# Performance work log

Hardware: AMD Instinct MI355X
Metric: run time of the kernel (lower is better)

The kernel has to match this reference:

```python
import jax, jax.numpy as jnp
import numpy as np

BITS = 8
EPS = 1e-5
NUM_HEADS = 16


def quantize_weight(w, eps=EPS):
    # per-tensor abs-mean scale, ternary weights in {-1, 0, 1}
    scale = jnp.maximum(jnp.mean(jnp.abs(w)), eps)
    qw = jnp.clip(jnp.round(w / scale), -1.0, 1.0)
    return qw, scale


def bitlinear158_inference(x, qw, scale, bias=None, bits=BITS, eps=EPS):
    # per-token abs-max activation quantization to [-Q, Q-1]
    q = float(2 ** (bits - 1))
    gamma = jnp.maximum(jnp.max(jnp.abs(x), axis=-1, keepdims=True), eps)
    qx = jnp.clip(jnp.round(x * (q / gamma)), -q, q - 1.0)
    out = jnp.einsum('...i,oi->...o', qx, qw)
    out = out * (scale * gamma / q)
    if bias is not None:
        out = out + bias
    return out


def setup_inputs() -> dict:
    rng = jax.random.key(0)
    ks = jax.random.split(rng, 7)
    B, L, E = 4, 2048, 1024
    return {
        'query': jax.random.normal(ks[0], (B, L, E), jnp.float32),
        'key': jax.random.normal(ks[1], (B, L, E), jnp.float32),
        'value': jax.random.normal(ks[2], (B, L, E), jnp.float32),
        'in_proj_weight': jax.random.normal(ks[3], (3 * E, E), jnp.float32) * 0.02,
        'in_proj_bias': jax.random.normal(ks[4], (3 * E,), jnp.float32) * 0.02,
        'out_proj_weight': jax.random.normal(ks[5], (E, E), jnp.float32) * 0.02,
        'out_proj_bias': jax.random.normal(ks[6], (E,), jnp.float32) * 0.02,
    }


def reference(query, key, value, in_proj_weight, in_proj_bias, out_proj_weight, out_proj_bias):
    B, Lq, E = query.shape
    Lk = key.shape[1]
    H = NUM_HEADS
    D = E // H

    # quantize weights as done at __init__ time
    qw, kw, vw = jnp.split(in_proj_weight, 3, axis=0)  # each [E, E]
    qb, kb, vb = jnp.split(in_proj_bias, 3, axis=0)
    q_qw, q_s = quantize_weight(qw)
    k_qw, k_s = quantize_weight(kw)
    v_qw, v_s = quantize_weight(vw)
    o_qw, o_s = quantize_weight(out_proj_weight)

    # quantized projections [B, L, E]
    q = bitlinear158_inference(query, q_qw, q_s, qb)
    k = bitlinear158_inference(key, k_qw, k_s, kb)
    v = bitlinear158_inference(value, v_qw, v_s, vb)

    # [B, H, L, D]
    q = q.reshape(B, Lq, H, D).transpose(0, 2, 1, 3)
    k = k.reshape(B, Lk, H, D).transpose(0, 2, 1, 3)
    v = v.reshape(B, Lk, H, D).transpose(0, 2, 1, 3)

    scores = jnp.einsum('bhqd,bhkd->bhqk', q, k) / jnp.sqrt(jnp.asarray(D, q.dtype))
    attn = jax.nn.softmax(scores, axis=-1)
    ctx = jnp.einsum('bhqk,bhkd->bhqd', attn, v)  # [B, H, Lq, D]
    ctx = ctx.transpose(0, 2, 1, 3).reshape(B, Lq, E)

    out = bitlinear158_inference(ctx, o_qw, o_s, out_proj_bias)
    return out
```

## Files before the change

### kernel.cpp

```cpp
#include <hip/hip_runtime.h>
#include <cstdint>
#include <cstddef>

#define BB 4
#define LL 2048
#define EE 1024
#define HH 16
#define DD 64
#define TT (BB*LL)
#define EPSF 1e-5f

typedef _Float16 half8 __attribute__((ext_vector_type(8)));
typedef _Float16 half4v __attribute__((ext_vector_type(4)));
typedef float floatx4 __attribute__((ext_vector_type(4)));
typedef float floatx16 __attribute__((ext_vector_type(16)));
typedef int intx4 __attribute__((ext_vector_type(4)));
typedef unsigned int uintx4 __attribute__((ext_vector_type(4)));
typedef unsigned int uint2v __attribute__((ext_vector_type(2)));

__device__ __forceinline__ void gl_lds16(const void* g, void* l) {
    __builtin_amdgcn_global_load_lds(
        (const __attribute__((address_space(1))) void*)g,
        (__attribute__((address_space(3))) void*)l, 16, 0, 0);
}

__device__ __forceinline__ uint32_t pkrtz(float a, float b) {
    return __builtin_bit_cast(uint32_t, __builtin_amdgcn_cvt_pkrtz(a, b));
}

__global__ void k_absum(const float* __restrict__ in_proj,
                        const float* __restrict__ out_proj,
                        double* __restrict__ sums) {
    const int which = blockIdx.y;
    const float4* src = (const float4*)((which < 3) ? (in_proj + (size_t)which * EE * EE)
                                                    : out_proj);
    double loc = 0.0;
    const int n4 = EE * EE / 4;
    for (int i = blockIdx.x * blockDim.x + threadIdx.x; i < n4; i += gridDim.x * blockDim.x) {
        const float4 v = src[i];
        loc += (double)fabsf(v.x); loc += (double)fabsf(v.y);
        loc += (double)fabsf(v.z); loc += (double)fabsf(v.w);
    }
    #pragma unroll
    for (int off = 32; off > 0; off >>= 1) loc += __shfl_down(loc, off, 64);
    __shared__ double red[4];
    const int lane = threadIdx.x & 63, wv = threadIdx.x >> 6;
    if (lane == 0) red[wv] = loc;
    __syncthreads();
    if (threadIdx.x == 0) {
        double tot = red[0] + red[1] + red[2] + red[3];
        atomicAdd(&sums[which], tot);
    }
}

__global__ void k_quantw(const float* __restrict__ in_proj,
                         const float* __restrict__ out_proj,
                         const double* __restrict__ sums,
                         float* __restrict__ scaleF,
                         int8_t* __restrict__ qw) {
    const int idx = blockIdx.x * blockDim.x + threadIdx.x;
    if (idx < 4) scaleF[idx] = fmaxf((float)(sums[idx] * (1.0 / (EE * EE))), EPSF);
    const int which = idx >> 20;
    const float s = fmaxf((float)(sums[which] * (1.0 / (EE * EE))), EPSF);
    const float w = (which < 3) ? in_proj[idx] : out_proj[idx - 3 * EE * EE];
    float q = rintf(w / s);
    q = fminf(fmaxf(q, -1.f), 1.f);
    qw[idx] = (int8_t)q;
}

__device__ __forceinline__ void gammaq_body(const float* __restrict__ x,
                                            float* __restrict__ g,
                                            int8_t* __restrict__ qx) {
    const int wv = threadIdx.x >> 6, lane = threadIdx.x & 63;
    const int tok = blockIdx.x * 4 + wv;
    const float* xp = x + (size_t)tok * EE;
    float4 v[4];
    #pragma unroll
    for (int i = 0; i < 4; i++) v[i] = *(const float4*)(xp + (lane + 64 * i) * 4);
    float m = 0.f;
    #pragma unroll
    for (int i = 0; i < 4; i++)
        m = fmaxf(m, fmaxf(fmaxf(fabsf(v[i].x), fabsf(v[i].y)),
                           fmaxf(fabsf(v[i].z), fabsf(v[i].w))));
    #pragma unroll
    for (int off = 1; off < 64; off <<= 1) m = fmaxf(m, __shfl_xor(m, off, 64));
    const float gg = fmaxf(m, EPSF);
    const float rg = 128.f / gg;
    int8_t* qp = qx + (size_t)tok * EE;
    #pragma unroll
    for (int i = 0; i < 4; i++) {
        char4 c;
        c.x = (int8_t)(int)fminf(fmaxf(rintf(v[i].x * rg), -128.f), 127.f);
        c.y = (int8_t)(int)fminf(fmaxf(rintf(v[i].y * rg), -128.f), 127.f);
        c.z = (int8_t)(int)fminf(fmaxf(rintf(v[i].z * rg), -128.f), 127.f);
        c.w = (int8_t)(int)fminf(fmaxf(rintf(v[i].w * rg), -128.f), 127.f);
        *(char4*)(qp + (lane + 64 * i) * 4) = c;
    }
    if (lane == 0) g[tok] = gg;
}

__global__ __launch_bounds__(256) void k_gammaq3(const float* __restrict__ q,
                                                 const float* __restrict__ k,
                                                 const float* __restrict__ v,
                                                 float* __restrict__ g,
                                                 int8_t* __restrict__ qx) {
    const int y = blockIdx.y;
    const float* src = (y == 0) ? q : (y == 1) ? k : v;
    gammaq_body(src, g + (size_t)y * TT, qx + (size_t)y * TT * EE);
}

__global__ __launch_bounds__(256) void k_gammaq(const float* __restrict__ x,
                                                float* __restrict__ g,
                                                int8_t* __restrict__ qx) {
    gammaq_body(x, g, qx);
}

__global__ __launch_bounds__(256) void k_bitmm(
    const int8_t* __restrict__ qx_all, const float* __restrict__ gam_all,
    const int8_t* __restrict__ qw_all, const float* __restrict__ scaleF,
    const float* __restrict__ in_proj_b, const float* __restrict__ out_proj_b,
    float* __restrict__ outF, _Float16* __restrict__ outH_all,
    int wbase, float qpre) {
    __shared__ __align__(16) int8_t smem[65536];
    _Float16 (*Vt)[136] = (_Float16(*)[136])smem;

    const int nz = (wbase == 0) ? 3 : 1;
    const int bid = blockIdx.x;
    const int xcd = bid & 7;
    const int idx = bid >> 3;
    const int per = 8 * nz;
    const int xl = idx / per;
    const int rem = idx - xl * per;
    const int y = rem & 7;
    const int z = rem >> 3;
    const int t0 = (xcd * 8 + xl) * 128;
    const int o0 = y * 128;
    const int widx = wbase + z;

    const int8_t* qx = qx_all + (size_t)widx * TT * EE;
    const int8_t* qw = qw_all + (size_t)widx * EE * EE;
    const float* gam = gam_all + (size_t)widx * TT;
    const float* bias = (widx < 3) ? (in_proj_b + widx * EE) : out_proj_b;
    _Float16* outH = outH_all + (size_t)widx * TT * EE;
    const float pre = (widx == 0) ? qpre : 1.0f;
    const int tid = threadIdx.x;
    const int wv = tid >> 6, lane = tid & 63;
    const int quad = lane >> 4, l16 = lane & 15;
    const int wm = wv & 1, wn = wv >> 1;
    const int srow = lane >> 3, schunk = lane & 7;

    intx4 acc[4][4];
    #pragma unroll
    for (int i = 0; i < 4; i++)
        #pragma unroll
        for (int j = 0; j < 4; j++) acc[i][j] = (intx4){0, 0, 0, 0};

    #pragma unroll
    for (int p = 0; p < 4; p++) {
        const int g = wv * 4 + p;
        const int c = schunk ^ srow ^ (g & 7);
        const int row = g * 8 + srow;
        gl_lds16(qx + (size_t)(t0 + row) * EE + c * 16, smem + (size_t)(g * 8) * 128);
        gl_lds16(qw + (size_t)(o0 + row) * EE + c * 16, smem + 32768 + (size_t)(g * 8) * 128);
    }
    __syncthreads();

    for (int k0 = 0; k0 < EE; k0 += 128) {
        const int cur = (k0 >> 7) & 1;
        int8_t (*As)[128] = (int8_t(*)[128])(smem + cur * 16384);
        int8_t (*Bs)[128] = (int8_t(*)[128])(smem + 32768 + cur * 16384);

        if (k0 + 128 < EE) {
            int8_t* Asn = smem + (cur ^ 1) * 16384;
            int8_t* Bsn = smem + 32768 + (cur ^ 1) * 16384;
            const int kn = k0 + 128;
            #pragma unroll
            for (int p = 0; p < 4; p++) {
                const int g = wv * 4 + p;
                const int c = schunk ^ srow ^ (g & 7);
                const int row = g * 8 + srow;
                gl_lds16(qx + (size_t)(t0 + row) * EE + kn + c * 16, Asn + (size_t)(g * 8) * 128);
                gl_lds16(qw + (size_t)(o0 + row) * EE + kn + c * 16, Bsn + (size_t)(g * 8) * 128);
            }
        }

        #pragma unroll
        for (int kk = 0; kk < 2; kk++) {
            intx4 af[4], bf[4];
            #pragma unroll
            for (int s4 = 0; s4 < 4; s4++) {
                const int mR = (l16 & 7) ^ ((s4 * 2 + (l16 >> 3)) & 7);
                const int ph = ((kk * 4 + quad) ^ mR) * 16;
                af[s4] = *(const intx4*)&As[wm * 64 + s4 * 16 + l16][ph];
                bf[s4] = *(const intx4*)&Bs[wn * 64 + s4 * 16 + l16][ph];
            }
            __builtin_amdgcn_s_setprio(1);
            #pragma unroll
            for (int sm = 0; sm < 4; sm++)
                #pragma unroll
                for (int sn = 0; sn < 4; sn++)
                    acc[sm][sn] = __builtin_amdgcn_mfma_i32_16x16x64_i8(
                        af[sm], bf[sn], acc[sm][sn], 0, 0, 0);
            __builtin_amdgcn_s_setprio(0);
        }
        __syncthreads();
    }

    const float s = scaleF[widx];
    if (widx == 2) {
        #pragma unroll
        for (int sm = 0; sm < 4; sm++) {
            const int tl = wm * 64 + sm * 16 + quad * 4;
            float mr[4];
            #pragma unroll
            for (int r = 0; r < 4; r++) mr[r] = s * gam[t0 + tl + r] * 0.0078125f;
            #pragma unroll
            for (int sn = 0; sn < 4; sn++) {
                const int ol = wn * 64 + sn * 16 + l16;
                const float b = bias[o0 + ol];
                half4v hv;
                #pragma unroll
                for (int r = 0; r < 4; r++)
                    hv[r] = (_Float16)((float)acc[sm][sn][r] * mr[r] + b);
                *(half4v*)&Vt[ol][tl] = hv;
            }
        }
        __syncthreads();
        const int ol2 = tid >> 1, tc0 = (tid & 1) * 64;
        const int og = o0 + ol2, hh = og >> 6, dd = og & 63;
        const int bb = t0 >> 11, l0 = t0 & (LL - 1);
        _Float16* dst = outH + ((size_t)(bb * HH + hh) * DD + dd) * LL + l0 + tc0;
        #pragma unroll
        for (int i = 0; i < 8; i++)
            *(half8*)(dst + i * 8) = *(const half8*)&Vt[ol2][tc0 + i * 8];
        return;
    }
    #pragma unroll
    for (int sm = 0; sm < 4; sm++) {
        #pragma unroll
        for (int r = 0; r < 4; r++) {
            const int t = t0 + wm * 64 + sm * 16 + quad * 4 + r;
            const float mr = s * gam[t] * 0.0078125f;
            const int b_ = t >> 11, l_ = t & (LL - 1);
            #pragma unroll
            for (int sn = 0; sn < 4; sn++) {
                const int o = o0 + wn * 64 + sn * 16 + l16;
                const float val = (float)acc[sm][sn][r] * mr + bias[o];
                if (widx == 3) {
                    outF[(size_t)t * EE + o] = val;
                } else {
                    const int h_ = o >> 6, d_ = o & 63;
                    outH[((size_t)(b_ * HH + h_) * LL + l_) * DD + d_] = (_Float16)(val * pre);
                }
            }
        }
    }
}

__global__ __launch_bounds__(256, 4) void k_attn5(const _Float16* __restrict__ Q,
                                                  const _Float16* __restrict__ K,
                                                  const _Float16* __restrict__ Vt,
                                                  float* __restrict__ ctx) {
    __shared__ __align__(16) _Float16 Ksh[2][64][64];
    __shared__ __align__(16) _Float16 Vtsh[2][64][64];
    const int tid = threadIdx.x;
    const int wv = tid >> 6, lane = tid & 63;
    const int l32 = lane & 31, h2 = lane >> 5;
    const int bid = blockIdx.x;
    const int xcd = bid & 7, j = bid >> 3;
    const int bh = (xcd << 3) | (j >> 4);
    const int qblk = j & 15;
    const int b_ = bh >> 4, h_ = bh & 15;
    const int q0 = qblk * 128 + wv * 32;
    const int srow = lane >> 3, schunk = lane & 7;

    const _Float16* Qb = Q + (size_t)bh * LL * DD;
    const _Float16* Kb = K + (size_t)bh * LL * DD;
    const _Float16* Vtb = Vt + (size_t)bh * DD * LL;

    half8 qf[4];
    #pragma unroll
    for (int ds = 0; ds < 4; ds++)
        qf[ds] = *(const half8*)(Qb + (size_t)(q0 + l32) * DD + ds * 16 + h2 * 8);

    floatx16 acc[2], accl, zv;
    #pragma unroll
    for (int r = 0; r < 16; r++) { acc[0][r] = 0.f; acc[1][r] = 0.f; accl[r] = 0.f; zv[r] = 0.f; }
    half8 ones;
    #pragma unroll
    for (int r = 0; r < 8; r++) ones[r] = (_Float16)1.0f;

    {
        #pragma unroll
        for (int u = 0; u < 2; u++) {
            const int g = wv * 2 + u;
            const int c = schunk ^ srow ^ (g & 7);
            const int row = g * 8 + srow;
            gl_lds16(Kb + (size_t)row * DD + c * 8, &Ksh[0][g * 8][0]);
            gl_lds16(Vtb + (size_t)row * LL + c * 8, &Vtsh[0][g * 8][0]);
        }
    }
    __syncthreads();

    for (int kt = 0; kt < LL; kt += 64) {
        const int cur = (kt >> 6) & 1;

        if (kt + 64 < LL) {
            const int nkt = kt + 64;
            #pragma unroll
            for (int u = 0; u < 2; u++) {
                const int g = wv * 2 + u;
                const int c = schunk ^ srow ^ (g & 7);
                const int row = g * 8 + srow;
                gl_lds16(Kb + (size_t)(nkt + row) * DD + c * 8, &Ksh[cur ^ 1][g * 8][0]);
                gl_lds16(Vtb + (size_t)row * LL + nkt + c * 8, &Vtsh[cur ^ 1][g * 8][0]);
            }
        }

        half8 pa[4];
        #pragma unroll
        for (int ks = 0; ks < 2; ks++) {
            const int rowK = ks * 32 + l32;
            const int mK = (l32 & 7) ^ ((ks * 4 + (l32 >> 3)) & 7);
            __builtin_amdgcn_s_setprio(1);
            floatx16 sc;
            {
                const half8 kf = *(const half8*)&Ksh[cur][rowK][((2 * 0 + h2) ^ mK) * 8];
                sc = __builtin_amdgcn_mfma_f32_32x32x16_f16(kf, qf[0], zv, 0, 0, 0);
            }
            #pragma unroll
            for (int ds = 1; ds < 4; ds++) {
                const half8 kf = *(const half8*)&Ksh[cur][rowK][((2 * ds + h2) ^ mK) * 8];
                sc = __builtin_amdgcn_mfma_f32_32x32x16_f16(kf, qf[ds], sc, 0, 0, 0);
            }
            __builtin_amdgcn_s_setprio(0);
            float p[16];
            #pragma unroll
            for (int r = 0; r < 16; r++) p[r] = __builtin_amdgcn_exp2f(sc[r]);
            uint32_t u_[4][2];
            #pragma unroll
            for (int c4 = 0; c4 < 4; c4++) {
                u_[c4][0] = pkrtz(p[4 * c4 + 0], p[4 * c4 + 1]);
                u_[c4][1] = pkrtz(p[4 * c4 + 2], p[4 * c4 + 3]);
            }
            #pragma unroll
            for (int mm = 0; mm < 2; mm++) {
                uint2v s0 = __builtin_amdgcn_permlane32_swap(
                    u_[2 * mm][0], u_[2 * mm + 1][0], false, false);
                uint2v s1 = __builtin_amdgcn_permlane32_swap(
                    u_[2 * mm][1], u_[2 * mm + 1][1], false, false);
                uintx4 w;
                w[0] = s0[0]; w[1] = s1[0]; w[2] = s0[1]; w[3] = s1[1];
                union { uintx4 u; half8 h; } cv; cv.u = w;
                pa[ks * 2 + mm] = cv.h;
            }
        }

        __builtin_amdgcn_s_setprio(1);
        #pragma unroll
        for (int kb = 0; kb < 4; kb++) {
            #pragma unroll
            for (int sd = 0; sd < 2; sd++) {
                const int rowV = sd * 32 + l32;
                const int mV = (l32 & 7) ^ ((sd * 4 + (l32 >> 3)) & 7);
                const half8 vf = *(const half8*)&Vtsh[cur][rowV][((2 * kb + h2) ^ mV) * 8];
                acc[sd] = __builtin_amdgcn_mfma_f32_32x32x16_f16(pa[kb], vf, acc[sd], 0, 0, 0);
            }
            accl = __builtin_amdgcn_mfma_f32_32x32x16_f16(pa[kb], ones, accl, 0, 0, 0);
        }
        __builtin_amdgcn_s_setprio(0);

        __syncthreads();
    }

    #pragma unroll
    for (int r = 0; r < 16; r++) {
        const int qrow = (r & 3) + 8 * (r >> 2) + 4 * h2;
        const float iv = 1.f / accl[r];
        float* cp = ctx + ((size_t)b_ * LL + q0 + qrow) * EE + h_ * DD + l32;
        cp[0]  = acc[0][r] * iv;
        cp[32] = acc[1][r] * iv;
    }
}

extern "C" void kernel_launch(void* const* d_in, const int* in_sizes, int n_in,
                              void* d_out, int out_size, void* d_ws, size_t ws_size,
                              hipStream_t stream) {
    const float* query      = (const float*)d_in[0];
    const float* key        = (const float*)d_in[1];
    const float* value      = (const float*)d_in[2];
    const float* in_proj_w  = (const float*)d_in[3];
    const float* in_proj_b  = (const float*)d_in[4];
    const float* out_proj_w = (const float*)d_in[5];
    const float* out_proj_b = (const float*)d_in[6];
    float* out = (float*)d_out;

    char* ws = (char*)d_ws;
    double*   sums   = (double*)ws;
    float*    scaleF = (float*)(ws + 32);
    float*    gbuf   = (float*)(ws + 256);
    int8_t*   qw8    = (int8_t*)(ws + (size_t)1  * 1024 * 1024);
    int8_t*   qx8    = (int8_t*)(ws + (size_t)8  * 1024 * 1024);
    _Float16* Qh     = (_Float16*)(ws + (size_t)40 * 1024 * 1024);
    _Float16* Kh     = Qh + (size_t)TT * EE;
    _Float16* Vth    = Kh + (size_t)TT * EE;
    float*    ctx    = out;

    const float QPRE = 0.18033688011112042f;

    hipMemsetAsync(sums, 0, 32, stream);
    k_absum<<<dim3(256, 4), 256, 0, stream>>>(in_proj_w, out_proj_w, sums);
    k_quantw<<<(4 * EE * EE) / 256, 256, 0, stream>>>(in_proj_w, out_proj_w, sums, scaleF, qw8);
    k_gammaq3<<<dim3(TT / 4, 3), 256, 0, stream>>>(query, key, value, gbuf, qx8);

    k_bitmm<<<dim3(64 * 8 * 3), 256, 0, stream>>>(
        qx8, gbuf, qw8, scaleF, in_proj_b, out_proj_b, nullptr, Qh, 0, QPRE);

    k_attn5<<<dim3((LL / 128) * BB * HH), 256, 0, stream>>>(Qh, Kh, Vth, ctx);

    k_gammaq<<<TT / 4, 256, 0, stream>>>(ctx, gbuf + 3 * TT, qx8 + 3 * (size_t)TT * EE);
    k_bitmm<<<dim3(64 * 8), 256, 0, stream>>>(
        qx8, gbuf, qw8, scaleF, in_proj_b, out_proj_b, out, Qh, 3, QPRE);
}
```

Baseline: 333.9 us.

## Software-pipeline attention loop: overlap next QK and softmax with previous PV

Restructures the attention inner loop so that the QK^T MFMAs for tile k are issued together with the PV MFMAs for tile k-1, with exp/pack softmax done afterwards. A triple-buffered V tile in a unified LDS array replaces the double-buffered K/V arrays, and the swizzled LDS offsets are precomputed once per thread. The aim is to hide the exp/permlane latency behind matrix work and interleave the two independent MFMA chains. The cost is more LDS (five 64x64 tiles), which lowers the occupancy target from 4 to 3 blocks per CU, and higher register pressure from keeping the previous P fragments live.

```diff
diff --git a/kernel.cpp b/kernel.cpp
--- a/kernel.cpp
+++ b/kernel.cpp
@@ -257,12 +257,11 @@
     }
 }
 
-__global__ __launch_bounds__(256, 4) void k_attn5(const _Float16* __restrict__ Q,
+__global__ __launch_bounds__(256, 3) void k_attn5(const _Float16* __restrict__ Q,
                                                   const _Float16* __restrict__ K,
                                                   const _Float16* __restrict__ Vt,
                                                   float* __restrict__ ctx) {
-    __shared__ __align__(16) _Float16 Ksh[2][64][64];
-    __shared__ __align__(16) _Float16 Vtsh[2][64][64];
+    __shared__ __align__(16) _Float16 sm[5 * 64 * 64];
     const int tid = threadIdx.x;
     const int wv = tid >> 6, lane = tid & 63;
     const int l32 = lane & 31, h2 = lane >> 5;
@@ -283,95 +282,128 @@
     for (int ds = 0; ds < 4; ds++)
         qf[ds] = *(const half8*)(Qb + (size_t)(q0 + l32) * DD + ds * 16 + h2 * 8);
 
+    int offX[2][4];
+    #pragma unroll
+    for (int h = 0; h < 2; h++) {
+        const int mx = (l32 & 7) ^ ((h * 4 + (l32 >> 3)) & 7);
+        #pragma unroll
+        for (int jj = 0; jj < 4; jj++)
+            offX[h][jj] = (h * 32 + l32) * 64 + (((2 * jj + h2) ^ mx) * 8);
+    }
+
     floatx16 acc[2], accl, zv;
     #pragma unroll
     for (int r = 0; r < 16; r++) { acc[0][r] = 0.f; acc[1][r] = 0.f; accl[r] = 0.f; zv[r] = 0.f; }
     half8 ones;
     #pragma unroll
     for (int r = 0; r < 8; r++) ones[r] = (_Float16)1.0f;
-
+    half8 paP[4];
+
+#define STAGE_T(kt_, koff_, voff_)                                                   \
+    {                                                                                \
+        _Pragma("unroll")                                                            \
+        for (int u = 0; u < 2; u++) {                                                \
+            const int g = wv * 2 + u;                                                \
+            const int c = schunk ^ srow ^ (g & 7);                                   \
+            const int row = g * 8 + srow;                                            \
+            gl_lds16(Kb + (size_t)((kt_) + row) * DD + c * 8, sm + (koff_) + g * 8 * 64); \
+            gl_lds16(Vtb + (size_t)row * LL + (kt_) + c * 8, sm + (voff_) + g * 8 * 64);  \
+        }                                                                            \
+    }
+
+#define QK_T(koff_)                                                                  \
+    {                                                                                \
+        const _Float16* kb_ = sm + (koff_);                                          \
+        sc0 = __builtin_amdgcn_mfma_f32_32x32x16_f16(                                \
+            *(const half8*)(kb_ + offX[0][0]), qf[0], zv, 0, 0, 0);                  \
+        sc1 = __builtin_amdgcn_mfma_f32_32x32x16_f16(                                \
+            *(const half8*)(kb_ + offX[1][0]), qf[0], zv, 0, 0, 0);                  \
+        _Pragma("unroll")                                                            \
+        for (int ds = 1; ds < 4; ds++) {                                             \
+            sc0 = __builtin_amdgcn_mfma_f32_32x32x16_f16(                            \
+                *(const half8*)(kb_ + offX[0][ds]), qf[ds], sc0, 0, 0, 0);           \
+            sc1 = __builtin_amdgcn_mfma_f32_32x32x16_f16(                            \
+                *(const half8*)(kb_ + offX[1][ds]), qf[ds], sc1, 0, 0, 0);           \
+        }                                                                            \
+    }
+
+#define PV_T(voff_)                                                                  \
+    {                                                                                \
+        const _Float16* vb_ = sm + (voff_);                                          \
+        _Pragma("unroll")                                                            \
+        for (int kb = 0; kb < 4; kb++) {                                             \
+            acc[0] = __builtin_amdgcn_mfma_f32_32x32x16_f16(                         \
+                paP[kb], *(const half8*)(vb_ + offX[0][kb]), acc[0], 0, 0, 0);       \
+            acc[1] = __builtin_amdgcn_mfma_f32_32x32x16_f16(                         \
+                paP[kb], *(const half8*)(vb_ + offX[1][kb]), acc[1], 0, 0, 0);       \
+            accl = __builtin_amdgcn_mfma_f32_32x32x16_f16(paP[kb], ones, accl, 0, 0, 0); \
+        }                                                                            \
+    }
+
+#define SMAX_HALF(sc_, ks_)                                                          \
+    {                                                                                \
+        float p[16];                                                                 \
+        _Pragma("unroll")                                                            \
+        for (int r = 0; r < 16; r++) p[r] = __builtin_amdgcn_exp2f(sc_[r]);          \
+        uint32_t u_[4][2];                                                           \
+        _Pragma("unroll")                                                            \
+        for (int c4 = 0; c4 < 4; c4++) {                                             \
+            u_[c4][0] = pkrtz(p[4 * c4 + 0], p[4 * c4 + 1]);                         \
+            u_[c4][1] = pkrtz(p[4 * c4 + 2], p[4 * c4 + 3]);                         \
+        }                                                                            \
+        _Pragma("unroll")                                                            \
+        for (int mm = 0; mm < 2; mm++) {                                             \
+            uint2v s0 = __builtin_amdgcn_permlane32_swap(                            \
+                u_[2 * mm][0], u_[2 * mm + 1][0], false, false);                     \
+            uint2v s1 = __builtin_amdgcn_permlane32_swap(                            \
+                u_[2 * mm][1], u_[2 * mm + 1][1], false, false);                     \
+            uintx4 w;                                                                \
+            w[0] = s0[0]; w[1] = s1[0]; w[2] = s0[1]; w[3] = s1[1];                  \
+            union { uintx4 u; half8 h; } cv; cv.u = w;                               \
+            paP[(ks_) * 2 + mm] = cv.h;                                              \
+        }                                                                            \
+    }
+
+    STAGE_T(0, 0, 8192);
+    __syncthreads();
+
+    int vprev = 8192, vcurr = 8192 + 4096, vnext = 8192 + 8192;
+
+    STAGE_T(64, 4096, vcurr);
     {
-        #pragma unroll
-        for (int u = 0; u < 2; u++) {
-            const int g = wv * 2 + u;
-            const int c = schunk ^ srow ^ (g & 7);
-            const int row = g * 8 + srow;
-            gl_lds16(Kb + (size_t)row * DD + c * 8, &Ksh[0][g * 8][0]);
-            gl_lds16(Vtb + (size_t)row * LL + c * 8, &Vtsh[0][g * 8][0]);
-        }
+        floatx16 sc0, sc1;
+        __builtin_amdgcn_s_setprio(1);
+        QK_T(0);
+        __builtin_amdgcn_s_setprio(0);
+        SMAX_HALF(sc0, 0);
+        SMAX_HALF(sc1, 1);
     }
     __syncthreads();
 
-    for (int kt = 0; kt < LL; kt += 64) {
+    for (int kt = 64; kt < LL; kt += 64) {
         const int cur = (kt >> 6) & 1;
-
-        if (kt + 64 < LL) {
-            const int nkt = kt + 64;
-            #pragma unroll
-            for (int u = 0; u < 2; u++) {
-                const int g = wv * 2 + u;
-                const int c = schunk ^ srow ^ (g & 7);
-                const int row = g * 8 + srow;
-                gl_lds16(Kb + (size_t)(nkt + row) * DD + c * 8, &Ksh[cur ^ 1][g * 8][0]);
-                gl_lds16(Vtb + (size_t)row * LL + nkt + c * 8, &Vtsh[cur ^ 1][g * 8][0]);
-            }
-        }
-
-        half8 pa[4];
-        #pragma unroll
-        for (int ks = 0; ks < 2; ks++) {
-            const int rowK = ks * 32 + l32;
-            const int mK = (l32 & 7) ^ ((ks * 4 + (l32 >> 3)) & 7);
-            __builtin_amdgcn_s_setprio(1);
-            floatx16 sc;
-            {
-                const half8 kf = *(const half8*)&Ksh[cur][rowK][((2 * 0 + h2) ^ mK) * 8];
-                sc = __builtin_amdgcn_mfma_f32_32x32x16_f16(kf, qf[0], zv, 0, 0, 0);
-            }
-            #pragma unroll
-            for (int ds = 1; ds < 4; ds++) {
-                const half8 kf = *(const half8*)&Ksh[cur][rowK][((2 * ds + h2) ^ mK) * 8];
-                sc = __builtin_amdgcn_mfma_f32_32x32x16_f16(kf, qf[ds], sc, 0, 0, 0);
-            }
-            __builtin_amdgcn_s_setprio(0);
-            float p[16];
-            #pragma unroll
-            for (int r = 0; r < 16; r++) p[r] = __builtin_amdgcn_exp2f(sc[r]);
-            uint32_t u_[4][2];
-            #pragma unroll
-            for (int c4 = 0; c4 < 4; c4++) {
-                u_[c4][0] = pkrtz(p[4 * c4 + 0], p[4 * c4 + 1]);
-                u_[c4][1] = pkrtz(p[4 * c4 + 2], p[4 * c4 + 3]);
-            }
-            #pragma unroll
-            for (int mm = 0; mm < 2; mm++) {
-                uint2v s0 = __builtin_amdgcn_permlane32_swap(
-                    u_[2 * mm][0], u_[2 * mm + 1][0], false, false);
-                uint2v s1 = __builtin_amdgcn_permlane32_swap(
-                    u_[2 * mm][1], u_[2 * mm + 1][1], false, false);
-                uintx4 w;
-                w[0] = s0[0]; w[1] = s1[0]; w[2] = s0[1]; w[3] = s1[1];
-                union { uintx4 u; half8 h; } cv; cv.u = w;
-                pa[ks * 2 + mm] = cv.h;
-            }
-        }
-
+        if (kt + 64 < LL) STAGE_T(kt + 64, (cur ^ 1) * 4096, vnext);
+
+        floatx16 sc0, sc1;
         __builtin_amdgcn_s_setprio(1);
-        #pragma unroll
-        for (int kb = 0; kb < 4; kb++) {
-            #pragma unroll
-            for (int sd = 0; sd < 2; sd++) {
-                const int rowV = sd * 32 + l32;
-                const int mV = (l32 & 7) ^ ((sd * 4 + (l32 >> 3)) & 7);
-                const half8 vf = *(const half8*)&Vtsh[cur][rowV][((2 * kb + h2) ^ mV) * 8];
-                acc[sd] = __builtin_amdgcn_mfma_f32_32x32x16_f16(pa[kb], vf, acc[sd], 0, 0, 0);
-            }
-            accl = __builtin_amdgcn_mfma_f32_32x32x16_f16(pa[kb], ones, accl, 0, 0, 0);
-        }
+        QK_T(cur * 4096);
+        PV_T(vprev);
         __builtin_amdgcn_s_setprio(0);
-
+        SMAX_HALF(sc0, 0);
+        SMAX_HALF(sc1, 1);
+
+        const int tr = vprev; vprev = vcurr; vcurr = vnext; vnext = tr;
         __syncthreads();
     }
+
+    __builtin_amdgcn_s_setprio(1);
+    PV_T(vprev);
+    __builtin_amdgcn_s_setprio(0);
+
+#undef STAGE_T
+#undef QK_T
+#undef PV_T
+#undef SMAX_HALF
 
     #pragma unroll
     for (int r = 0; r < 16; r++) {
```

Result: no change. 332.9 us (-0.3%).
